# Kernel optimization log

Hardware: AMD Instinct MI355X
Metric: run time of the kernel (lower is better)

The kernel has to match this reference:

```python
import jax, jax.numpy as jnp
import numpy as np

B, N, C_SA, OUT = 16, 2048, 512, 1024
BN_EPS = 1e-5


def pconv(x, w, b=None):
    # 1x1 Conv1d: x [B,Cin,N], w [Cout,Cin] -> [B,Cout,N]
    y = jnp.einsum('oc,bcn->bon', w, x)
    return y if b is None else y + b[None, :, None]


def setup_inputs() -> dict:
    key = jax.random.key(0)
    ks = jax.random.split(key, 16)
    s = lambda k, shape: jax.random.normal(k, shape, dtype=jnp.float32) * 0.05
    return {
        'x': jax.random.normal(ks[0], (B, 3, N), dtype=jnp.float32),
        'w1': s(ks[1], (128, 21)), 'b1': s(ks[2], (128,)),
        'w2': s(ks[3], (256, 128)), 'b2': s(ks[4], (256,)),
        'w3': s(ks[5], (512, 512)), 'b3': s(ks[6], (512,)),
        'w4': s(ks[7], (OUT, 512)), 'b4': s(ks[8], (OUT,)),
        'wqk': s(ks[9], (C_SA // 4, C_SA)),            # q_conv.weight tied to k_conv.weight, no bias
        'wv': s(ks[10], (C_SA, C_SA)), 'bv': s(ks[11], (C_SA,)),
        'wt': s(ks[12], (C_SA, C_SA)), 'bt': s(ks[13], (C_SA,)),
        'gamma': jnp.ones((C_SA,), dtype=jnp.float32),
        'beta': jnp.zeros((C_SA,), dtype=jnp.float32),
    }


def reference(x, w1, b1, w2, b2, w3, b3, w4, b4, wqk, wv, bv, wt, bt, gamma, beta):
    b, _, n = x.shape
    # positional encoding on [B,N,3]: [t, sin(t*2^i), cos(t*2^i)] for i in 0..2 -> 21 channels
    t = jnp.transpose(x, (0, 2, 1))
    enc = [t]
    for f in (1.0, 2.0, 4.0):
        enc.append(jnp.sin(t * f))
        enc.append(jnp.cos(t * f))
    h = jnp.transpose(jnp.concatenate(enc, axis=-1), (0, 2, 1))  # [B,21,N]

    h = jax.nn.relu(pconv(h, w1, b1))               # [B,128,N]
    h = pconv(h, w2, b2)                            # [B,256,N]
    g = jnp.max(h, axis=2)                          # [B,256]
    h = jnp.concatenate([h, jnp.broadcast_to(g[:, :, None], (b, g.shape[1], n))], axis=1)  # [B,512,N]
    h = jax.nn.relu(pconv(h, w3, b3))               # [B,512,N]

    # SA_Layer (offset attention, double normalization)
    xq = jnp.einsum('oc,bcn->bno', wqk, h)          # [B,N,128]
    xk = jnp.einsum('oc,bcn->bon', wqk, h)          # [B,128,N]
    xv = pconv(h, wv, bv)                           # [B,512,N]
    energy = jnp.einsum('bqo,bok->bqk', xq, xk)     # [B,N,N]
    attn = jax.nn.softmax(energy, axis=-1)
    attn = attn / (1e-9 + jnp.sum(attn, axis=1, keepdims=True))  # L1 renorm over query dim
    x_r = jnp.einsum('bck,bqk->bcq', xv, attn)      # x_v @ attn^T -> [B,512,N]
    d = pconv(h - x_r, wt, bt)
    # BatchNorm1d, training mode (batch statistics, biased variance)
    mu = jnp.mean(d, axis=(0, 2))
    var = jnp.var(d, axis=(0, 2))
    d = gamma[None, :, None] * (d - mu[None, :, None]) * jax.lax.rsqrt(var + BN_EPS)[None, :, None] + beta[None, :, None]
    h = h + jax.nn.relu(d)

    h = pconv(h, w4, b4)                            # [B,OUT,N]
    return jnp.max(h, axis=2)                       # [B,OUT]
```

## Files before the change

kernel.cpp:

```cpp
#include <hip/hip_runtime.h>
#include <cmath>

#define GN 2048
#define GB 16

typedef __attribute__((ext_vector_type(8))) short bf8_t;
typedef __attribute__((ext_vector_type(4))) float f4_t;

__device__ __forceinline__ short f2bf(float f) {
    union { float f; unsigned u; } v; v.f = f;
    unsigned r = v.u + 0x7FFFu + ((v.u >> 16) & 1u);
    return (short)(r >> 16);
}
__device__ __forceinline__ float bf2f(short s) {
    union { unsigned u; float f; } v; v.u = ((unsigned)(unsigned short)s) << 16;
    return v.f;
}

__device__ __forceinline__ void load16_lds(const short* g, short* l) {
    __builtin_amdgcn_global_load_lds(
        (const __attribute__((address_space(1))) unsigned int*)g,
        (__attribute__((address_space(3))) unsigned int*)l, 16, 0, 0);
}

__device__ __forceinline__ float wave_sum(float v) {
#pragma unroll
    for (int o = 32; o > 0; o >>= 1) v += __shfl_xor(v, o, 64);
    return v;
}
__device__ __forceinline__ float block_sum(float v) {
    __shared__ float sm[4];
    v = wave_sum(v);
    if ((threadIdx.x & 63) == 0) sm[threadIdx.x >> 6] = v;
    __syncthreads();
    v = sm[0] + sm[1] + sm[2] + sm[3];
    __syncthreads();
    return v;
}

__global__ __launch_bounds__(256) void f2ball_k(
    const float* __restrict__ w2, const float* __restrict__ w3,
    const float* __restrict__ wqk, const float* __restrict__ wv,
    const float* __restrict__ wt, const float* __restrict__ w4,
    short* __restrict__ dst) {
    int i = blockIdx.x * 256 + threadIdx.x;
    if (i >= 1409024) return;
    float v;
    if (i < 32768) v = w2[i];
    else if (i < 294912) v = w3[i - 32768];
    else if (i < 360448) v = wqk[i - 294912];
    else if (i < 622592) v = wv[i - 360448];
    else if (i < 884736) v = wt[i - 622592];
    else v = w4[i - 884736];
    dst[i] = f2bf(v);
}

__global__ __launch_bounds__(256) void posenc_conv1_k(
    const float* __restrict__ x, const float* __restrict__ w1,
    const float* __restrict__ b1, short* __restrict__ h1) {
    __shared__ float w[128 * 21];
    __shared__ float bb[128];
    __shared__ float se[128][21];
    const int tid = threadIdx.x;
    for (int i = tid; i < 128 * 21; i += 256) w[i] = w1[i];
    if (tid < 128) bb[tid] = b1[tid];
    int p0 = blockIdx.x * 128;
    if (tid < 128) {
        int p = p0 + tid, b = p >> 11, n = p & (GN - 1);
        const float* xb = x + (long)b * 3 * GN + n;
        float t0 = xb[0], t1 = xb[GN], t2 = xb[2 * GN];
        se[tid][0] = t0; se[tid][1] = t1; se[tid][2] = t2;
        se[tid][3] = sinf(t0); se[tid][4] = sinf(t1); se[tid][5] = sinf(t2);
        se[tid][6] = cosf(t0); se[tid][7] = cosf(t1); se[tid][8] = cosf(t2);
        se[tid][9] = sinf(2.f * t0); se[tid][10] = sinf(2.f * t1); se[tid][11] = sinf(2.f * t2);
        se[tid][12] = cosf(2.f * t0); se[tid][13] = cosf(2.f * t1); se[tid][14] = cosf(2.f * t2);
        se[tid][15] = sinf(4.f * t0); se[tid][16] = sinf(4.f * t1); se[tid][17] = sinf(4.f * t2);
        se[tid][18] = cosf(4.f * t0); se[tid][19] = cosf(4.f * t1); se[tid][20] = cosf(4.f * t2);
    }
    __syncthreads();
    short* outb = h1 + (long)p0 * 128;
    for (int it = 0; it < 64; ++it) {
        int L = it * 256 + tid;
        int pl = L >> 7, o = L & 127;
        float s = bb[o];
        const float* er = se[pl];
        const float* wr = &w[o * 21];
#pragma unroll
        for (int c = 0; c < 21; ++c) s = fmaf(wr[c], er[c], s);
        outb[L] = f2bf(fmaxf(s, 0.f));
    }
}

template <int MODE, int BIAS, bool RELU, bool STATS = false, bool COLMAX = false>
__global__ __launch_bounds__(256) void mm_k(
    const short* __restrict__ A, int lda, long long aB,
    const short* __restrict__ B, int ldb, long long bB,
    const float* __restrict__ bias, int biasStride,
    const short* __restrict__ aux, long long auxB,
    const float* __restrict__ rsv,
    float* __restrict__ Cf, long long cfB,
    short* __restrict__ Cb, long long cbB,
    float* __restrict__ Pmax, float* __restrict__ Ps2,
    int ldc, int K) {
    const int z = blockIdx.z;
    A += (long long)z * aB;
    B += (long long)z * bB;
    if (MODE == 4) { aux += (long long)z * auxB; rsv += (long long)z * GN; }
    if (MODE == 1) Cf += (long long)z * cfB;
    if (MODE == 2 || MODE == 4 || MODE == 6) Cb += (long long)z * cbB;
    if (MODE == 6) Pmax += (long long)z * GN * 32;
    const int row0 = blockIdx.x * 128, col0 = blockIdx.y * 128;
    const int tid = threadIdx.x;
    const int lane = tid & 63, w = tid >> 6;
    const int r = lane & 15, q = lane >> 4;
    const int wr = w >> 1, wc = w & 1;

    __shared__ short lA[8192];
    __shared__ short lB[8192];

    f4_t acc[4][4] = {};

    const int sRow = lane >> 2;
    const int sKb = (lane & 3) ^ ((lane >> 3) & 3);
    const long aG = (long)(row0 + w * 32 + sRow) * lda + sKb * 8;
    const long bG = (long)(col0 + w * 32 + sRow) * ldb + sKb * 8;
    short* ldsA0 = lA + (w * 32) * 32;
    short* ldsA1 = lA + (w * 32 + 16) * 32;
    short* ldsB0 = lB + (w * 32) * 32;
    short* ldsB1 = lB + (w * 32 + 16) * 32;

    const int sw = (q ^ ((r >> 1) & 3)) * 8;
    int aoff[4], boff[4];
#pragma unroll
    for (int i = 0; i < 4; ++i) {
        aoff[i] = (wr * 64 + i * 16 + r) * 32 + sw;
        boff[i] = (wc * 64 + i * 16 + r) * 32 + sw;
    }

    for (int k0 = 0; k0 < K; k0 += 64) {
        __syncthreads();
        load16_lds(A + aG + k0, ldsA0);
        load16_lds(A + aG + (long)16 * lda + k0, ldsA1);
        load16_lds(B + bG + k0, ldsB0);
        load16_lds(B + bG + (long)16 * ldb + k0, ldsB1);
        load16_lds(A + aG + k0 + 32, ldsA0 + 4096);
        load16_lds(A + aG + (long)16 * lda + k0 + 32, ldsA1 + 4096);
        load16_lds(B + bG + k0 + 32, ldsB0 + 4096);
        load16_lds(B + bG + (long)16 * ldb + k0 + 32, ldsB1 + 4096);
        asm volatile("s_waitcnt vmcnt(0)" ::: "memory");
        __syncthreads();
#pragma unroll
        for (int h = 0; h < 2; ++h) {
            const short* la = lA + h * 4096;
            const short* lb = lB + h * 4096;
            bf8_t av[4], bv[4];
#pragma unroll
            for (int i = 0; i < 4; ++i) av[i] = *(const bf8_t*)(la + aoff[i]);
#pragma unroll
            for (int j = 0; j < 4; ++j) bv[j] = *(const bf8_t*)(lb + boff[j]);
#pragma unroll
            for (int i = 0; i < 4; ++i)
#pragma unroll
                for (int j = 0; j < 4; ++j)
                    acc[i][j] = __builtin_amdgcn_mfma_f32_16x16x32_bf16(av[i], bv[j], acc[i][j], 0, 0, 0);
        }
    }

    if constexpr (MODE == 5) {
        int b = row0 >> 11;
        int rw = (blockIdx.x * 2 + wr) & 31;
#pragma unroll
        for (int j = 0; j < 4; ++j) {
            float vm = -1e30f;
#pragma unroll
            for (int i = 0; i < 4; ++i)
#pragma unroll
                for (int e = 0; e < 4; ++e) vm = fmaxf(vm, acc[i][j][e]);
            vm = fmaxf(vm, __shfl_xor(vm, 16, 64));
            vm = fmaxf(vm, __shfl_xor(vm, 32, 64));
            if (q == 0) {
                int gcol = col0 + wc * 64 + j * 16 + r;
                Pmax[(((long)b * 1024 + gcol) << 5) + rw] = vm + bias[gcol];
            }
        }
    } else if constexpr (MODE == 6) {
        float rsum[4][4] = {};
#pragma unroll
        for (int j = 0; j < 4; ++j) {
            int gcol = col0 + wc * 64 + j * 16 + r;
#pragma unroll
            for (int i = 0; i < 4; ++i) {
#pragma unroll
                for (int e = 0; e < 4; ++e) {
                    int grow = row0 + wr * 64 + i * 16 + q * 4 + e;
                    float ex = __expf(acc[i][j][e]);
                    rsum[i][e] += ex;
                    Cb[(long)grow * ldc + gcol] = f2bf(ex);
                }
            }
        }
#pragma unroll
        for (int i = 0; i < 4; ++i)
#pragma unroll
            for (int e = 0; e < 4; ++e) {
                float v = rsum[i][e];
                v += __shfl_xor(v, 1, 64);
                v += __shfl_xor(v, 2, 64);
                v += __shfl_xor(v, 4, 64);
                v += __shfl_xor(v, 8, 64);
                if (r == 0) {
                    int grow = row0 + wr * 64 + i * 16 + q * 4 + e;
                    Pmax[((long)grow << 5) + blockIdx.y * 2 + wc] = v;
                }
            }
    } else if constexpr (MODE == 4) {
#pragma unroll
        for (int i = 0; i < 4; ++i) {
#pragma unroll
            for (int e = 0; e < 4; ++e) {
                int grow = row0 + wr * 64 + i * 16 + q * 4 + e;
                float rsr = rsv[grow];
                long ob = (long)grow * ldc + col0 + wc * 64 + r;
#pragma unroll
                for (int j = 0; j < 4; ++j) {
                    long off = ob + j * 16;
                    Cb[off] = f2bf(bf2f(aux[off]) - acc[i][j][e] * rsr);
                }
            }
        }
    } else {
        const int b2d = (BIAS == 3) ? (row0 >> 11) : 0;
#pragma unroll
        for (int j = 0; j < 4; ++j) {
            int gcol = col0 + wc * 64 + j * 16 + r;
            float bvv = 0.f;
            if constexpr (BIAS == 1) bvv = bias[gcol];
            if constexpr (BIAS == 3) bvv = bias[b2d * biasStride + gcol];
            float s1 = 0.f, s2 = 0.f;
            float cmx = -1e30f;
#pragma unroll
            for (int i = 0; i < 4; ++i) {
#pragma unroll
                for (int e = 0; e < 4; ++e) {
                    int grow = row0 + wr * 64 + i * 16 + q * 4 + e;
                    float v = acc[i][j][e] + bvv;
                    if constexpr (BIAS == 2) v += bias[grow];
                    if constexpr (RELU) v = fmaxf(v, 0.f);
                    if constexpr (STATS) { s1 += v; s2 = fmaf(v, v, s2); }
                    if constexpr (COLMAX) cmx = fmaxf(cmx, v);
                    long off = (long)grow * ldc + gcol;
                    if constexpr (MODE == 1) Cf[off] = v;
                    if constexpr (MODE == 2) Cb[off] = f2bf(v);
                }
            }
            if constexpr (STATS) {
                s1 += __shfl_xor(s1, 16, 64); s1 += __shfl_xor(s1, 32, 64);
                s2 += __shfl_xor(s2, 16, 64); s2 += __shfl_xor(s2, 32, 64);
                if (q == 0) {
                    int rw2 = blockIdx.x * 2 + wr;
                    Pmax[rw2 * 512 + gcol] = s1;
                    Ps2[rw2 * 512 + gcol] = s2;
                }
            }
            if constexpr (COLMAX) {
                cmx = fmaxf(cmx, __shfl_xor(cmx, 16, 64));
                cmx = fmaxf(cmx, __shfl_xor(cmx, 32, 64));
                if (q == 0) {
                    int b = row0 >> 11;
                    int rw = (blockIdx.x * 2 + wr) & 31;
                    Pmax[(((long)b * ldc + gcol) << 5) + rw] = cmx;
                }
            }
        }
    }
}

__device__ __forceinline__ void stage2(const short* g0, const short* g1, short* dst) {
    load16_lds(g0, dst);
    load16_lds(g1, dst + 4096);
}

template <int MH, int NH>
__device__ __forceinline__ void mfma_quad(const bf8_t (&av)[4][2], const bf8_t (&bv)[2][2],
                                          f4_t (&acc)[8][4]) {
#pragma unroll
    for (int mi = 0; mi < 4; ++mi)
#pragma unroll
        for (int ni = 0; ni < 2; ++ni) {
            acc[MH * 4 + mi][NH * 2 + ni] = __builtin_amdgcn_mfma_f32_16x16x32_bf16(
                av[mi][0], bv[ni][0], acc[MH * 4 + mi][NH * 2 + ni], 0, 0, 0);
            acc[MH * 4 + mi][NH * 2 + ni] = __builtin_amdgcn_mfma_f32_16x16x32_bf16(
                av[mi][1], bv[ni][1], acc[MH * 4 + mi][NH * 2 + ni], 0, 0, 0);
        }
}

__device__ __forceinline__ void rd4(const short* p, int swz0, int swz1, bf8_t (&v)[4][2]) {
#pragma unroll
    for (int i = 0; i < 4; ++i) {
        v[i][0] = *(const bf8_t*)(p + i * 1024 + swz0);
        v[i][1] = *(const bf8_t*)(p + i * 1024 + swz1);
    }
}
__device__ __forceinline__ void rd2(const short* p, int swz0, int swz1, bf8_t (&v)[2][2]) {
#pragma unroll
    for (int i = 0; i < 2; ++i) {
        v[i][0] = *(const bf8_t*)(p + i * 1024 + swz0);
        v[i][1] = *(const bf8_t*)(p + i * 1024 + swz1);
    }
}

#define SB0 __builtin_amdgcn_sched_barrier(0)
#define BARRIER asm volatile("s_barrier" ::: "memory")

template <int MODE, int BIAS, bool RELU, bool STATS = false>
__global__ __launch_bounds__(512, 2) void mm256_k(
    const short* __restrict__ A, int lda, long long aB,
    const short* __restrict__ B, int ldb, long long bB,
    const float* __restrict__ bias, int biasStride,
    const short* __restrict__ aux, long long auxB,
    const float* __restrict__ rsv,
    short* __restrict__ Cb, long long cbB,
    float* __restrict__ Pmax, float* __restrict__ Ps2,
    int ldc, int K) {
    __shared__ short lA[32768];
    __shared__ short lB[32768];
    const int bx = blockIdx.x, by = blockIdx.y, bz = blockIdx.z;
    const int z = bz;
    A += (long long)z * aB;
    B += (long long)z * bB;
    if constexpr (MODE == 4) { aux += (long long)z * auxB; rsv += (long long)z * GN; }
    if constexpr (MODE != 5) Cb += (long long)z * cbB;
    if constexpr (MODE == 6) Pmax += (long long)z * GN * 32;
    const int row0 = bx * 256, col0 = by * 256;
    const int tid = threadIdx.x;
    const int lane = tid & 63, w = tid >> 6;
    const int r16 = lane & 15, q = lane >> 4;
    const int wr = w >> 2, wc = w & 3;

    const int rc0 = w * 8 + (lane >> 3);
    const int s8 = ((lane & 7) ^ (rc0 & 7)) * 8;
    const long ldA64 = (long)64 * lda, ldB64 = (long)64 * ldb;
    const short* aH0 = A + (long)(row0 + rc0) * lda + s8;
    const short* aH1 = aH0 + (long)128 * lda;
    const short* bH0 = B + (long)(col0 + rc0) * ldb + s8;
    const short* bH1 = bH0 + (long)128 * ldb;
    short* dA = lA + w * 512;
    short* dB = lB + w * 512;

#define STG_A(d_, h_, kt_) stage2((h_ ? aH1 : aH0) + (long)(kt_) * 64,                      \
                                  (h_ ? aH1 : aH0) + (long)(kt_) * 64 + ldA64,              \
                                  dA + (d_) * 16384 + (h_) * 8192)
#define STG_B(d_, h_, kt_) stage2((h_ ? bH1 : bH0) + (long)(kt_) * 64,                      \
                                  (h_ ? bH1 : bH0) + (long)(kt_) * 64 + ldB64,              \
                                  dB + (d_) * 16384 + (h_) * 8192)

    const int swz0 = (q ^ (r16 & 7)) * 8;
    const int swz1 = ((4 + q) ^ (r16 & 7)) * 8;
    const int arow = (wr * 64 + r16) * 64;
    const int brow = (wc * 32 + r16) * 64;

    f4_t acc[8][4] = {};
    bf8_t av[4][2], bv0[2][2], bv1[2][2];
    const int NT = K >> 6;

    STG_A(0, 0, 0); STG_B(0, 0, 0); STG_A(0, 1, 0); STG_B(0, 1, 0);
    if (NT > 1) {
        STG_A(1, 0, 1); STG_B(1, 0, 1);
        asm volatile("s_waitcnt vmcnt(4)" ::: "memory");
    } else {
        asm volatile("s_waitcnt vmcnt(0)" ::: "memory");
    }
    BARRIER; SB0;

    for (int t = 0; t < NT; ++t) {
        const int d = t & 1;
        const short* la = lA + d * 16384;
        const short* lb = lB + d * 16384;
        rd4(la + arow, swz0, swz1, av);
        rd2(lb + brow, swz0, swz1, bv0);
        rd2(lb + 8192 + brow, swz0, swz1, bv1);
        if (t + 1 < NT) { STG_A(d ^ 1, 1, t + 1); STG_B(d ^ 1, 1, t + 1); }
        __builtin_amdgcn_s_setprio(1);
        mfma_quad<0, 0>(av, bv0, acc);
        mfma_quad<0, 1>(av, bv1, acc);
        __builtin_amdgcn_s_setprio(0);
        BARRIER; SB0;
        rd4(la + 8192 + arow, swz0, swz1, av);
        if (t + 2 < NT) { STG_A(d, 0, t + 2); STG_B(d, 0, t + 2); }
        __builtin_amdgcn_s_setprio(1);
        mfma_quad<1, 0>(av, bv0, acc);
        mfma_quad<1, 1>(av, bv1, acc);
        __builtin_amdgcn_s_setprio(0);
        if (t + 2 < NT) {
            asm volatile("s_waitcnt vmcnt(4)" ::: "memory");
        } else if (t + 1 < NT) {
            asm volatile("s_waitcnt vmcnt(0)" ::: "memory");
        }
        BARRIER; SB0;
    }
#undef STG_A
#undef STG_B

    const int mrow = row0 + wr * 64 + q * 4;
    const int ncol = col0 + wc * 32 + r16;

    if constexpr (MODE == 4) {
#pragma unroll
        for (int m = 0; m < 8; ++m) {
#pragma unroll
            for (int e = 0; e < 4; ++e) {
                const int grow = mrow + (m >> 2) * 128 + (m & 3) * 16 + e;
                const float rsr = rsv[grow];
                const long rb = (long)grow * ldc;
#pragma unroll
                for (int n = 0; n < 4; ++n) {
                    const long off = rb + ncol + (n >> 1) * 128 + (n & 1) * 16;
                    Cb[off] = f2bf(bf2f(aux[off]) - acc[m][n][e] * rsr);
                }
            }
        }
    } else if constexpr (MODE == 6) {
        float rsum[8][4] = {};
#pragma unroll
        for (int n = 0; n < 4; ++n) {
            const int gcol = ncol + (n >> 1) * 128 + (n & 1) * 16;
#pragma unroll
            for (int m = 0; m < 8; ++m) {
#pragma unroll
                for (int e = 0; e < 4; ++e) {
                    const int grow = mrow + (m >> 2) * 128 + (m & 3) * 16 + e;
                    float ex = __expf(acc[m][n][e]);
                    rsum[m][e] += ex;
                    Cb[(long)grow * ldc + gcol] = f2bf(ex);
                }
            }
        }
#pragma unroll
        for (int m = 0; m < 8; ++m)
#pragma unroll
            for (int e = 0; e < 4; ++e) {
                float v = rsum[m][e];
                v += __shfl_xor(v, 1, 64);
                v += __shfl_xor(v, 2, 64);
                v += __shfl_xor(v, 4, 64);
                v += __shfl_xor(v, 8, 64);
                if (r16 == 0) {
                    const int grow = mrow + (m >> 2) * 128 + (m & 3) * 16 + e;
                    Pmax[((long)grow << 5) + (by << 2) + wc] = v;
                }
            }
    } else if constexpr (MODE == 2) {
        const int b2d = (BIAS == 3) ? (row0 >> 11) : 0;
#pragma unroll
        for (int n = 0; n < 4; ++n) {
            const int gcol = ncol + (n >> 1) * 128 + (n & 1) * 16;
            float bvv = 0.f;
            if constexpr (BIAS == 1) bvv = bias[gcol];
            if constexpr (BIAS == 3) bvv = bias[b2d * biasStride + gcol];
#pragma unroll
            for (int mh = 0; mh < 2; ++mh) {
                float s1 = 0.f, s2 = 0.f;
#pragma unroll
                for (int mi = 0; mi < 4; ++mi) {
#pragma unroll
                    for (int e = 0; e < 4; ++e) {
                        const int grow = mrow + mh * 128 + mi * 16 + e;
                        float v = acc[mh * 4 + mi][n][e] + bvv;
                        if constexpr (BIAS == 2) v += bias[grow];
                        if constexpr (RELU) v = fmaxf(v, 0.f);
                        if constexpr (STATS) { s1 += v; s2 = fmaf(v, v, s2); }
                        Cb[(long)grow * ldc + gcol] = f2bf(v);
                    }
                }
                if constexpr (STATS) {
                    s1 += __shfl_xor(s1, 16, 64); s1 += __shfl_xor(s1, 32, 64);
                    s2 += __shfl_xor(s2, 16, 64); s2 += __shfl_xor(s2, 32, 64);
                    if (q == 0) {
                        const int rw2 = bx * 4 + mh * 2 + wr;
                        Pmax[rw2 * 512 + gcol] = s1;
                        Ps2[rw2 * 512 + gcol] = s2;
                    }
                }
            }
        }
    } else if constexpr (MODE == 5) {
        const int b = row0 >> 11;
#pragma unroll
        for (int n = 0; n < 4; ++n) {
            const int gcol = ncol + (n >> 1) * 128 + (n & 1) * 16;
            const float bvv = bias[gcol];
#pragma unroll
            for (int mh = 0; mh < 2; ++mh) {
                float vm = -1e30f;
#pragma unroll
                for (int mi = 0; mi < 4; ++mi)
#pragma unroll
                    for (int e = 0; e < 4; ++e) vm = fmaxf(vm, acc[mh * 4 + mi][n][e]);
                vm = fmaxf(vm, __shfl_xor(vm, 16, 64));
                vm = fmaxf(vm, __shfl_xor(vm, 32, 64));
                if (q == 0) {
                    const int rw = (bx * 4 + mh * 2 + wr) & 31;
                    Pmax[(((long)b * ldc + gcol) << 5) + rw] = vm + bvv;
                }
            }
        }
    }
}
#undef SB0
#undef BARRIER

__global__ __launch_bounds__(256) void rs_k(const float* __restrict__ rp,
                                            float* __restrict__ rs) {
    int i = blockIdx.x * 256 + threadIdx.x;
    const float* p = rp + ((long)i << 5);
    float s = 0.f;
#pragma unroll
    for (int j = 0; j < 32; ++j) s += p[j];
    rs[i] = 1.f / s;
}

__global__ __launch_bounds__(256) void maxg_k(const float* __restrict__ P,
                                              float* __restrict__ g) {
    int i = blockIdx.x * 256 + threadIdx.x;
    const float* p = P + ((long)i << 5);
    float m = p[0];
#pragma unroll
    for (int j = 1; j < 32; ++j) m = fmaxf(m, p[j]);
    g[i] = m;
}

__global__ __launch_bounds__(256) void cvec_k(const float* __restrict__ w3,
                                              const float* __restrict__ b3,
                                              const float* __restrict__ g,
                                              float* __restrict__ cvec) {
    int idx = blockIdx.x * 256 + threadIdx.x;
    int b = idx >> 9, o = idx & 511;
    const float* gb = g + (b << 8);
    const float* wr = w3 + (long)o * 512 + 256;
    float s = b3[o];
    for (int c = 0; c < 256; ++c) s = fmaf(wr[c], gb[c], s);
    cvec[idx] = s;
}

__global__ __launch_bounds__(256) void colsum1_k(const short* __restrict__ Ab,
                                                 const float* __restrict__ rs,
                                                 float* __restrict__ cp) {
    const int qs = blockIdx.x, z = blockIdx.y;
    const int k0 = threadIdx.x * 8;
    const short* p = Ab + (long)z * GN * GN + (long)qs * 64 * GN + k0;
    const float* rv = rs + z * GN + qs * 64;
    float s[8] = {};
    for (int qq = 0; qq < 64; ++qq) {
        uint4 v = *(const uint4*)(p + (long)qq * GN);
        const float rr = rv[qq];
        const short* sp = (const short*)&v;
#pragma unroll
        for (int j = 0; j < 8; ++j) s[j] = fmaf(bf2f(sp[j]), rr, s[j]);
    }
    float* o = cp + ((long)(z * 32 + qs) * GN) + k0;
#pragma unroll
    for (int j = 0; j < 8; ++j) o[j] = s[j];
}
__global__ __launch_bounds__(256) void colsum2_k(const float* __restrict__ cp,
                                                 float* __restrict__ cs) {
    int k = blockIdx.x * 256 + threadIdx.x, z = blockIdx.y;
    float s = 1e-9f;
    for (int qs = 0; qs < 32; ++qs) s += cp[((z * 32 + qs) * GN) + k];
    cs[z * GN + k] = s;
}

__global__ __launch_bounds__(256) void xvscale_k(short* __restrict__ xvc,
                                                 const float* __restrict__ cs) {
    long idx = ((long)blockIdx.x * 256 + threadIdx.x) * 8;
    int p = (int)(idx & 32767);
    short* ptr = xvc + idx;
    float4 c0 = *(const float4*)(cs + p);
    float4 c1 = *(const float4*)(cs + p + 4);
    uint4 u = *(const uint4*)ptr;
    short* sp = (short*)&u;
    sp[0] = f2bf(bf2f(sp[0]) / c0.x);
    sp[1] = f2bf(bf2f(sp[1]) / c0.y);
    sp[2] = f2bf(bf2f(sp[2]) / c0.z);
    sp[3] = f2bf(bf2f(sp[3]) / c0.w);
    sp[4] = f2bf(bf2f(sp[4]) / c1.x);
    sp[5] = f2bf(bf2f(sp[5]) / c1.y);
    sp[6] = f2bf(bf2f(sp[6]) / c1.z);
    sp[7] = f2bf(bf2f(sp[7]) / c1.w);
    *(uint4*)ptr = u;
}

__global__ __launch_bounds__(256) void bn2_k(const float* __restrict__ bs1,
                                             const float* __restrict__ bs2,
                                             const float* __restrict__ gamma,
                                             const float* __restrict__ beta,
                                             float* __restrict__ sc,
                                             float* __restrict__ sh) {
    int c = blockIdx.x;
    float s = 0.f, s2 = 0.f;
    for (int i = threadIdx.x; i < 512; i += 256) {
        s += bs1[i * 512 + c];
        s2 += bs2[i * 512 + c];
    }
    s = block_sum(s);
    s2 = block_sum(s2);
    if (threadIdx.x == 0) {
        const float cnt = (float)(GB * GN);
        float mu = s / cnt;
        float var = s2 / cnt - mu * mu;
        float r = rsqrtf(var + 1e-5f);
        float gm = gamma[c] * r;
        sc[c] = gm;
        sh[c] = beta[c] - gm * mu;
    }
}

__global__ __launch_bounds__(256) void bn_apply_k(const short* __restrict__ h3b,
                                                  const short* __restrict__ d,
                                                  const float* __restrict__ sc,
                                                  const float* __restrict__ sh,
                                                  short* __restrict__ h4) {
    long bidx = ((long)blockIdx.x * 256 + threadIdx.x) * 8;
    int c = (int)(bidx & 511);
    uint4 du = *(const uint4*)(d + bidx);
    short* ds = (short*)&du;
    uint4 hu = *(const uint4*)(h3b + bidx);
    short* hs = (short*)&hu;
    float4 a0 = *(const float4*)(sc + c);
    float4 a1 = *(const float4*)(sc + c + 4);
    float4 b0 = *(const float4*)(sh + c);
    float4 b1 = *(const float4*)(sh + c + 4);
    float r0 = bf2f(hs[0]) + fmaxf(fmaf(bf2f(ds[0]), a0.x, b0.x), 0.f);
    float r1 = bf2f(hs[1]) + fmaxf(fmaf(bf2f(ds[1]), a0.y, b0.y), 0.f);
    float r2 = bf2f(hs[2]) + fmaxf(fmaf(bf2f(ds[2]), a0.z, b0.z), 0.f);
    float r3 = bf2f(hs[3]) + fmaxf(fmaf(bf2f(ds[3]), a0.w, b0.w), 0.f);
    float r4 = bf2f(hs[4]) + fmaxf(fmaf(bf2f(ds[4]), a1.x, b1.x), 0.f);
    float r5 = bf2f(hs[5]) + fmaxf(fmaf(bf2f(ds[5]), a1.y, b1.y), 0.f);
    float r6 = bf2f(hs[6]) + fmaxf(fmaf(bf2f(ds[6]), a1.z, b1.z), 0.f);
    float r7 = bf2f(hs[7]) + fmaxf(fmaf(bf2f(ds[7]), a1.w, b1.w), 0.f);
    uint4 o;
    o.x = (unsigned short)f2bf(r0) | ((unsigned)(unsigned short)f2bf(r1) << 16);
    o.y = (unsigned short)f2bf(r2) | ((unsigned)(unsigned short)f2bf(r3) << 16);
    o.z = (unsigned short)f2bf(r4) | ((unsigned)(unsigned short)f2bf(r5) << 16);
    o.w = (unsigned short)f2bf(r6) | ((unsigned)(unsigned short)f2bf(r7) << 16);
    *(uint4*)(h4 + bidx) = o;
}

__global__ __launch_bounds__(256) void max_final_k(const float* __restrict__ P,
                                                   float* __restrict__ out) {
    int i = blockIdx.x * 256 + threadIdx.x;
    const float* p = P + ((long)i << 5);
    float m = p[0];
#pragma unroll
    for (int j = 1; j < 32; ++j) m = fmaxf(m, p[j]);
    out[i] = m;
}

extern "C" void kernel_launch(void* const* d_in, const int* in_sizes, int n_in,
                              void* d_out, int out_size, void* d_ws, size_t ws_size,
                              hipStream_t stream) {
    const float* x = (const float*)d_in[0];
    const float* w1 = (const float*)d_in[1];
    const float* b1 = (const float*)d_in[2];
    const float* w2 = (const float*)d_in[3];
    const float* b2 = (const float*)d_in[4];
    const float* w3 = (const float*)d_in[5];
    const float* b3 = (const float*)d_in[6];
    const float* w4 = (const float*)d_in[7];
    const float* b4 = (const float*)d_in[8];
    const float* wqk = (const float*)d_in[9];
    const float* wv = (const float*)d_in[10];
    const float* bv = (const float*)d_in[11];
    const float* wt = (const float*)d_in[12];
    const float* bt = (const float*)d_in[13];
    const float* gamma = (const float*)d_in[14];
    const float* beta = (const float*)d_in[15];
    float* out = (float*)d_out;

    char* base = (char*)d_ws;
    short* h3b = (short*)base;
    short* hsT = (short*)(base + 33554432);
    short* kT  = (short*)(base + 67108864);
    short* xvc = (short*)(base + 75497472);
    short* EA  = (short*)(base + 109051904);
    short* h1T = (short*)(base + 109051904);
    short* h2T = (short*)(base + 117440512);
    short* dTb = (short*)(base + 109051904);
    short* h4T = (short*)(base + 67108864);
    char* S = base + 243269632;
    float* g    = (float*)(S + 262144);
    float* cvec = (float*)(S + 278528);
    float* cp   = (float*)(S + 311296);
    float* rp   = cp;
    float* cs   = (float*)(S + 4505600);
    float* bs1  = (float*)(S + 4636672);
    float* bs2  = (float*)(S + 5685248);
    float* bnsc = (float*)(S + 6733824);
    float* bnsh = (float*)(S + 6735872);
    float* Pmax = (float*)(S + 6737920);
    short* w2b  = (short*)(S + 8835072);
    short* w3b  = (short*)(S + 8900608);
    short* wqkb = (short*)(S + 9424896);
    short* wvb  = (short*)(S + 9555968);
    short* wtb  = (short*)(S + 10080256);
    short* w4b  = (short*)(S + 10604544);
    float* rs   = (float*)(S + 11653120);

    f2ball_k<<<5505, 256, 0, stream>>>(w2, w3, wqk, wv, wt, w4, w2b);

    posenc_conv1_k<<<256, 256, 0, stream>>>(x, w1, b1, h1T);

    mm_k<2, 1, false, false, true><<<dim3(256, 2, 1), 256, 0, stream>>>(
        h1T, 128, 0, w2b, 128, 0, b2, 0, nullptr, 0, nullptr,
        nullptr, 0, h2T, 0, Pmax, nullptr, 256, 128);

    maxg_k<<<16, 256, 0, stream>>>(Pmax, g);

    cvec_k<<<32, 256, 0, stream>>>(w3, b3, g, cvec);

    mm_k<2, 3, true><<<dim3(256, 4, 1), 256, 0, stream>>>(
        h2T, 256, 0, w3b, 512, 0, cvec, 512, nullptr, 0, nullptr,
        nullptr, 0, h3b, 0, nullptr, nullptr, 512, 256);

    mm_k<2, 0, false><<<dim3(256, 1, 1), 256, 0, stream>>>(
        h3b, 512, 0, wqkb, 512, 0, nullptr, 0, nullptr, 0, nullptr,
        nullptr, 0, kT, 0, nullptr, nullptr, 128, 512);

    mm_k<2, 2, false><<<dim3(4, 256, 1), 256, 0, stream>>>(
        wvb, 512, 0, h3b, 512, 0, bv, 0, nullptr, 0, nullptr,
        nullptr, 0, xvc, 0, nullptr, nullptr, 32768, 512);

    mm_k<6, 0, false><<<dim3(16, 16, 16), 256, 0, stream>>>(
        kT, 128, (long long)GN * 128, kT, 128, (long long)GN * 128,
        nullptr, 0, nullptr, 0, nullptr, nullptr, 0,
        EA, (long long)GN * GN, rp, nullptr, GN, 128);
    rs_k<<<128, 256, 0, stream>>>(rp, rs);
    colsum1_k<<<dim3(32, GB), 256, 0, stream>>>(EA, rs, cp);
    colsum2_k<<<dim3(8, GB), 256, 0, stream>>>(cp, cs);
    xvscale_k<<<8192, 256, 0, stream>>>(xvc, cs);
    mm256_k<4, 0, false><<<dim3(8, 2, 16), 512, 0, stream>>>(
        EA, GN, (long long)GN * GN,
        xvc, 32768, (long long)GN,
        nullptr, 0, h3b, (long long)GN * 512, rs,
        hsT, (long long)GN * 512, nullptr, nullptr, 512, GN);

    mm256_k<2, 1, false, true><<<dim3(128, 2, 1), 512, 0, stream>>>(
        hsT, 512, 0, wtb, 512, 0, bt, 0, nullptr, 0, nullptr,
        dTb, 0, bs1, bs2, 512, 512);

    bn2_k<<<512, 256, 0, stream>>>(bs1, bs2, gamma, beta, bnsc, bnsh);

    bn_apply_k<<<8192, 256, 0, stream>>>(h3b, dTb, bnsc, bnsh, h4T);

    mm256_k<5, 1, false><<<dim3(128, 4, 1), 512, 0, stream>>>(
        h4T, 512, 0, w4b, 512, 0, b4, 0, nullptr, 0, nullptr,
        nullptr, 0, Pmax, nullptr, 1024, 512);

    max_final_k<<<64, 256, 0, stream>>>(Pmax, out);
}
```

Measured before the change: 521.8 us.

## Add K=128 specialized GEMM kernel and fuse global max with cvec computation

Adds a 128x128-tile GEMM kernel specialized for K=128 that stages the whole K dimension into LDS up front, waiting in two halves so the first half's MFMAs start before the second half arrives. The kernel replaces the generic looping mm_k for the conv2 layer (with column-max) and for the energy/exp attention GEMM. It also fuses the per-batch max reduction and the cvec matvec into one kernel, which removes one launch and the intermediate g buffer. The risk is a lower-occupancy single-shot load pattern and a 16-block fused matvec with less parallelism than the old 32-block cvec kernel.

```diff
diff --git a/kernel.cpp b/kernel.cpp
--- a/kernel.cpp
+++ b/kernel.cpp
@@ -275,6 +275,152 @@
     }
 }
 
+template <int MODE, int BIAS, bool RELU, bool STATS = false, bool COLMAX = false>
+__global__ __launch_bounds__(256) void mmk128_k(
+    const short* __restrict__ A, int lda, long long aB,
+    const short* __restrict__ B, int ldb, long long bB,
+    const float* __restrict__ bias,
+    short* __restrict__ Cb, long long cbB,
+    float* __restrict__ Pmax, float* __restrict__ Ps2,
+    int ldc) {
+    const int z = blockIdx.z;
+    A += (long long)z * aB;
+    B += (long long)z * bB;
+    if (MODE == 2 || MODE == 6) Cb += (long long)z * cbB;
+    if (MODE == 6) Pmax += (long long)z * GN * 32;
+    const int row0 = blockIdx.x * 128, col0 = blockIdx.y * 128;
+    const int tid = threadIdx.x;
+    const int lane = tid & 63, w = tid >> 6;
+    const int r = lane & 15, q = lane >> 4;
+    const int wr = w >> 1, wc = w & 1;
+
+    __shared__ short lA[16384];
+    __shared__ short lB[16384];
+
+    f4_t acc[4][4] = {};
+
+    const int sRow = lane >> 2;
+    const int sKb = (lane & 3) ^ ((lane >> 3) & 3);
+    const long aG = (long)(row0 + w * 32 + sRow) * lda + sKb * 8;
+    const long bG = (long)(col0 + w * 32 + sRow) * ldb + sKb * 8;
+    short* ldsA0 = lA + (w * 32) * 32;
+    short* ldsA1 = lA + (w * 32 + 16) * 32;
+    short* ldsB0 = lB + (w * 32) * 32;
+    short* ldsB1 = lB + (w * 32 + 16) * 32;
+
+    const int sw = (q ^ ((r >> 1) & 3)) * 8;
+    int aoff[4], boff[4];
+#pragma unroll
+    for (int i = 0; i < 4; ++i) {
+        aoff[i] = (wr * 64 + i * 16 + r) * 32 + sw;
+        boff[i] = (wc * 64 + i * 16 + r) * 32 + sw;
+    }
+
+#pragma unroll
+    for (int s = 0; s < 4; ++s) {
+        load16_lds(A + aG + s * 32, ldsA0 + s * 4096);
+        load16_lds(A + aG + (long)16 * lda + s * 32, ldsA1 + s * 4096);
+        load16_lds(B + bG + s * 32, ldsB0 + s * 4096);
+        load16_lds(B + bG + (long)16 * ldb + s * 32, ldsB1 + s * 4096);
+    }
+    asm volatile("s_waitcnt vmcnt(8)" ::: "memory");
+    asm volatile("s_barrier" ::: "memory");
+    __builtin_amdgcn_sched_barrier(0);
+#pragma unroll
+    for (int h = 0; h < 2; ++h) {
+        const short* la = lA + h * 4096;
+        const short* lb = lB + h * 4096;
+        bf8_t av[4], bv[4];
+#pragma unroll
+        for (int i = 0; i < 4; ++i) av[i] = *(const bf8_t*)(la + aoff[i]);
+#pragma unroll
+        for (int j = 0; j < 4; ++j) bv[j] = *(const bf8_t*)(lb + boff[j]);
+#pragma unroll
+        for (int i = 0; i < 4; ++i)
+#pragma unroll
+            for (int j = 0; j < 4; ++j)
+                acc[i][j] = __builtin_amdgcn_mfma_f32_16x16x32_bf16(av[i], bv[j], acc[i][j], 0, 0, 0);
+    }
+    asm volatile("s_waitcnt vmcnt(0)" ::: "memory");
+    asm volatile("s_barrier" ::: "memory");
+    __builtin_amdgcn_sched_barrier(0);
+#pragma unroll
+    for (int h = 2; h < 4; ++h) {
+        const short* la = lA + h * 4096;
+        const short* lb = lB + h * 4096;
+        bf8_t av[4], bv[4];
+#pragma unroll
+        for (int i = 0; i < 4; ++i) av[i] = *(const bf8_t*)(la + aoff[i]);
+#pragma unroll
+        for (int j = 0; j < 4; ++j) bv[j] = *(const bf8_t*)(lb + boff[j]);
+#pragma unroll
+        for (int i = 0; i < 4; ++i)
+#pragma unroll
+            for (int j = 0; j < 4; ++j)
+                acc[i][j] = __builtin_amdgcn_mfma_f32_16x16x32_bf16(av[i], bv[j], acc[i][j], 0, 0, 0);
+    }
+
+    if constexpr (MODE == 6) {
+        float rsum[4][4] = {};
+#pragma unroll
+        for (int j = 0; j < 4; ++j) {
+            int gcol = col0 + wc * 64 + j * 16 + r;
+#pragma unroll
+            for (int i = 0; i < 4; ++i) {
+#pragma unroll
+                for (int e = 0; e < 4; ++e) {
+                    int grow = row0 + wr * 64 + i * 16 + q * 4 + e;
+                    float ex = __expf(acc[i][j][e]);
+                    rsum[i][e] += ex;
+                    Cb[(long)grow * ldc + gcol] = f2bf(ex);
+                }
+            }
+        }
+#pragma unroll
+        for (int i = 0; i < 4; ++i)
+#pragma unroll
+            for (int e = 0; e < 4; ++e) {
+                float v = rsum[i][e];
+                v += __shfl_xor(v, 1, 64);
+                v += __shfl_xor(v, 2, 64);
+                v += __shfl_xor(v, 4, 64);
+                v += __shfl_xor(v, 8, 64);
+                if (r == 0) {
+                    int grow = row0 + wr * 64 + i * 16 + q * 4 + e;
+                    Pmax[((long)grow << 5) + blockIdx.y * 2 + wc] = v;
+                }
+            }
+    } else if constexpr (MODE == 2) {
+#pragma unroll
+        for (int j = 0; j < 4; ++j) {
+            int gcol = col0 + wc * 64 + j * 16 + r;
+            float bvv = 0.f;
+            if constexpr (BIAS == 1) bvv = bias[gcol];
+            float cmx = -1e30f;
+#pragma unroll
+            for (int i = 0; i < 4; ++i) {
+#pragma unroll
+                for (int e = 0; e < 4; ++e) {
+                    int grow = row0 + wr * 64 + i * 16 + q * 4 + e;
+                    float v = acc[i][j][e] + bvv;
+                    if constexpr (RELU) v = fmaxf(v, 0.f);
+                    if constexpr (COLMAX) cmx = fmaxf(cmx, v);
+                    Cb[(long)grow * ldc + gcol] = f2bf(v);
+                }
+            }
+            if constexpr (COLMAX) {
+                cmx = fmaxf(cmx, __shfl_xor(cmx, 16, 64));
+                cmx = fmaxf(cmx, __shfl_xor(cmx, 32, 64));
+                if (q == 0) {
+                    int b = row0 >> 11;
+                    int rw = (blockIdx.x * 2 + wr) & 31;
+                    Pmax[(((long)b * ldc + gcol) << 5) + rw] = cmx;
+                }
+            }
+        }
+    }
+}
+
 __device__ __forceinline__ void stage2(const short* g0, const short* g1, short* dst) {
     load16_lds(g0, dst);
     load16_lds(g1, dst + 4096);
@@ -330,7 +476,6 @@
     B += (long long)z * bB;
     if constexpr (MODE == 4) { aux += (long long)z * auxB; rsv += (long long)z * GN; }
     if constexpr (MODE != 5) Cb += (long long)z * cbB;
-    if constexpr (MODE == 6) Pmax += (long long)z * GN * 32;
     const int row0 = bx * 256, col0 = by * 256;
     const int tid = threadIdx.x;
     const int lane = tid & 63, w = tid >> 6;
@@ -419,36 +564,6 @@
                 }
             }
         }
-    } else if constexpr (MODE == 6) {
-        float rsum[8][4] = {};
-#pragma unroll
-        for (int n = 0; n < 4; ++n) {
-            const int gcol = ncol + (n >> 1) * 128 + (n & 1) * 16;
-#pragma unroll
-            for (int m = 0; m < 8; ++m) {
-#pragma unroll
-                for (int e = 0; e < 4; ++e) {
-                    const int grow = mrow + (m >> 2) * 128 + (m & 3) * 16 + e;
-                    float ex = __expf(acc[m][n][e]);
-                    rsum[m][e] += ex;
-                    Cb[(long)grow * ldc + gcol] = f2bf(ex);
-                }
-            }
-        }
-#pragma unroll
-        for (int m = 0; m < 8; ++m)
-#pragma unroll
-            for (int e = 0; e < 4; ++e) {
-                float v = rsum[m][e];
-                v += __shfl_xor(v, 1, 64);
-                v += __shfl_xor(v, 2, 64);
-                v += __shfl_xor(v, 4, 64);
-                v += __shfl_xor(v, 8, 64);
-                if (r16 == 0) {
-                    const int grow = mrow + (m >> 2) * 128 + (m & 3) * 16 + e;
-                    Pmax[((long)grow << 5) + (by << 2) + wc] = v;
-                }
-            }
     } else if constexpr (MODE == 2) {
         const int b2d = (BIAS == 3) ? (row0 >> 11) : 0;
 #pragma unroll
@@ -519,27 +634,27 @@
     rs[i] = 1.f / s;
 }
 
-__global__ __launch_bounds__(256) void maxg_k(const float* __restrict__ P,
-                                              float* __restrict__ g) {
-    int i = blockIdx.x * 256 + threadIdx.x;
-    const float* p = P + ((long)i << 5);
+__global__ __launch_bounds__(256) void maxg_cvec_k(const float* __restrict__ P,
+                                                   const float* __restrict__ w3,
+                                                   const float* __restrict__ b3,
+                                                   float* __restrict__ cvec) {
+    const int b = blockIdx.x;
+    __shared__ float gs[256];
+    const int c = threadIdx.x;
+    const float* p = P + ((long)(b * 256 + c) << 5);
     float m = p[0];
 #pragma unroll
     for (int j = 1; j < 32; ++j) m = fmaxf(m, p[j]);
-    g[i] = m;
-}
-
-__global__ __launch_bounds__(256) void cvec_k(const float* __restrict__ w3,
-                                              const float* __restrict__ b3,
-                                              const float* __restrict__ g,
-                                              float* __restrict__ cvec) {
-    int idx = blockIdx.x * 256 + threadIdx.x;
-    int b = idx >> 9, o = idx & 511;
-    const float* gb = g + (b << 8);
-    const float* wr = w3 + (long)o * 512 + 256;
-    float s = b3[o];
-    for (int c = 0; c < 256; ++c) s = fmaf(wr[c], gb[c], s);
-    cvec[idx] = s;
+    gs[c] = m;
+    __syncthreads();
+#pragma unroll
+    for (int t = 0; t < 2; ++t) {
+        const int o = t * 256 + threadIdx.x;
+        const float* wr = w3 + (long)o * 512 + 256;
+        float s = b3[o];
+        for (int cc = 0; cc < 256; ++cc) s = fmaf(wr[cc], gs[cc], s);
+        cvec[b * 512 + o] = s;
+    }
 }
 
 __global__ __launch_bounds__(256) void colsum1_k(const short* __restrict__ Ab,
@@ -687,7 +802,6 @@
     short* dTb = (short*)(base + 109051904);
     short* h4T = (short*)(base + 67108864);
     char* S = base + 243269632;
-    float* g    = (float*)(S + 262144);
     float* cvec = (float*)(S + 278528);
     float* cp   = (float*)(S + 311296);
     float* rp   = cp;
@@ -709,13 +823,10 @@
 
     posenc_conv1_k<<<256, 256, 0, stream>>>(x, w1, b1, h1T);
 
-    mm_k<2, 1, false, false, true><<<dim3(256, 2, 1), 256, 0, stream>>>(
-        h1T, 128, 0, w2b, 128, 0, b2, 0, nullptr, 0, nullptr,
-        nullptr, 0, h2T, 0, Pmax, nullptr, 256, 128);
-
-    maxg_k<<<16, 256, 0, stream>>>(Pmax, g);
-
-    cvec_k<<<32, 256, 0, stream>>>(w3, b3, g, cvec);
+    mmk128_k<2, 1, false, false, true><<<dim3(256, 2, 1), 256, 0, stream>>>(
+        h1T, 128, 0, w2b, 128, 0, b2, h2T, 0, Pmax, nullptr, 256);
+
+    maxg_cvec_k<<<16, 256, 0, stream>>>(Pmax, w3, b3, cvec);
 
     mm_k<2, 3, true><<<dim3(256, 4, 1), 256, 0, stream>>>(
         h2T, 256, 0, w3b, 512, 0, cvec, 512, nullptr, 0, nullptr,
@@ -729,10 +840,9 @@
         wvb, 512, 0, h3b, 512, 0, bv, 0, nullptr, 0, nullptr,
         nullptr, 0, xvc, 0, nullptr, nullptr, 32768, 512);
 
-    mm_k<6, 0, false><<<dim3(16, 16, 16), 256, 0, stream>>>(
+    mmk128_k<6, 0, false><<<dim3(16, 16, 16), 256, 0, stream>>>(
         kT, 128, (long long)GN * 128, kT, 128, (long long)GN * 128,
-        nullptr, 0, nullptr, 0, nullptr, nullptr, 0,
-        EA, (long long)GN * GN, rp, nullptr, GN, 128);
+        nullptr, EA, (long long)GN * GN, rp, nullptr, GN);
     rs_k<<<128, 256, 0, stream>>>(rp, rs);
     colsum1_k<<<dim3(32, GB), 256, 0, stream>>>(EA, rs, cp);
     colsum2_k<<<dim3(8, GB), 256, 0, stream>>>(cp, cs);
```

New measurement: 507.1 us. 1.03x faster.
